# Optimization experiments

Hardware: AMD Instinct MI355X
Metric: run time of the kernel (lower is better)

## Reference

```python
import jax, jax.numpy as jnp
import numpy as np

B, N, M, D = 2, 256, 8, 256      # batch, seq, modalities, dmodel
H, DH = 8, 64                     # heads, dim_head (hardcoded defaults)
INNER = H * DH                    # 512
MULT = 4                          # FFN mult
SCALE = DH ** -0.5
EPS = 1e-5


def layer_norm(x, g, b):
    mu = jnp.mean(x, axis=-1, keepdims=True)
    var = jnp.mean((x - mu) ** 2, axis=-1, keepdims=True)
    return (x - mu) * jax.lax.rsqrt(var + EPS) * g + b


def setup_inputs() -> dict:
    key = jax.random.key(0)
    ks = jax.random.split(key, 8)
    s = 0.02
    return {
        "x": jax.random.normal(ks[0], (B, D, M, N), jnp.float32),
        "Wq": jax.random.normal(ks[1], (D, INNER), jnp.float32) * s,
        "Wkv": jax.random.normal(ks[2], (D, 2 * INNER), jnp.float32) * s,
        "Wout": jax.random.normal(ks[3], (INNER * M, D * M), jnp.float32) * s,
        "bout": jnp.zeros((D * M,), jnp.float32),
        "g1": jnp.ones((D,), jnp.float32),
        "beta1": jnp.zeros((D,), jnp.float32),
        "Wff1": jax.random.normal(ks[4], (D, 2 * D * MULT), jnp.float32) * s,
        "bff1": jnp.zeros((2 * D * MULT,), jnp.float32),
        "Wff2": jax.random.normal(ks[5], (D * MULT, D), jnp.float32) * s,
        "bff2": jnp.zeros((D,), jnp.float32),
        "g2": jnp.ones((D,), jnp.float32),
        "beta2": jnp.zeros((D,), jnp.float32),
    }


def reference(x, Wq, Wkv, Wout, bout, g1, beta1, Wff1, bff1, Wff2, bff2, g2, beta2):
    x_shape = x.shape
    xt = jnp.transpose(x, (0, 3, 2, 1))          # [B,N,M,D]
    # --- Channel_Seq_Big_Attention (self-attention, context = x) ---
    q = (xt @ Wq).reshape(B, N, M, H, DH)
    kv = xt @ Wkv
    k, v = jnp.split(kv, 2, axis=-1)
    k = k.reshape(B, N, M, H, DH)
    v = v.reshape(B, N, M, H, DH)
    # sim: [(b h), i, j, m, z] kept as [B,H,i,j,m,z]
    sim = jnp.einsum('bimhd,bjzhd->bhijmz', q, k) * SCALE
    attn = jax.nn.softmax(sim, axis=2)           # softmax over j (dim=-3 of bijmz)
    out = jnp.einsum('bhijmz,bjmhd->bizhd', attn, v)  # [B,N,M,H,DH]
    out = out.reshape(B, N, M * H * DH)          # 'b n (m h d)'
    o = (out @ Wout + bout).reshape(B, N, M, D)
    # --- residual + post-norm ---
    xt = layer_norm(xt + o, g1, beta1)
    # --- GEGLU FFN ---
    hg = xt @ Wff1 + bff1
    a, gate = jnp.split(hg, 2, axis=-1)
    ff = (a * jax.nn.gelu(gate, approximate=False)) @ Wff2 + bff2
    xt = layer_norm(xt + ff, g2, beta2)
    return xt.reshape(x_shape)                   # torch .view(x_shape)
```

## Files before the change

### kernel.cpp

```cpp
#include <hip/hip_runtime.h>
#include <math.h>

#define KS_ 0.1803368801111244f

typedef __attribute__((ext_vector_type(8))) short bf16x8;
typedef __attribute__((ext_vector_type(4))) short bf16x4;
typedef __attribute__((ext_vector_type(4))) float f32x4;

__device__ inline short f2bf(float f) {
  unsigned u = __builtin_bit_cast(unsigned, f);
  u += 0x7fff + ((u >> 16) & 1);
  return (short)(u >> 16);
}

__device__ inline void wt_tile(const float* __restrict__ W, short* __restrict__ WT,
                               int K, int N, int bx, int by, int t, float (*tile)[33]) {
  int n0 = bx * 32, k0 = by * 32;
  int tx = t & 31, ty = t >> 5;
#pragma unroll
  for (int r = 0; r < 32; r += 8)
    tile[ty + r][tx] = W[(size_t)(k0 + ty + r) * N + n0 + tx];
  __syncthreads();
#pragma unroll
  for (int r = 0; r < 32; r += 8)
    WT[(size_t)(n0 + ty + r) * K + k0 + tx] = f2bf(tile[tx][ty + r]);
}

__global__ __launch_bounds__(256) void k_prep_all(const float* __restrict__ x, float* __restrict__ xt,
                                                  short* __restrict__ xtbf,
                                                  const float* __restrict__ Wq, const float* __restrict__ Wkv,
                                                  const float* __restrict__ Wout, const float* __restrict__ Wff1,
                                                  const float* __restrict__ Wff2,
                                                  short* __restrict__ WqkvT, short* __restrict__ WoutT,
                                                  short* __restrict__ Wff1T, short* __restrict__ Wff2T) {
  __shared__ float tile[32][33];
  int bid = blockIdx.x, t = threadIdx.x;
  if (bid < 8192) {
    wt_tile(Wout, WoutT, 4096, 2048, bid & 63, bid >> 6, t, tile);
  } else if (bid < 9216) {
    int r = bid - 8192;
    int bx = r & 7, by = (r >> 3) & 7, bm = r >> 6;
    int b = bm >> 3, m = bm & 7;
    int d0 = bx * 32, n0 = by * 32;
    int tx = t & 31, ty = t >> 5;
#pragma unroll
    for (int rr = 0; rr < 32; rr += 8) {
      int d = d0 + ty + rr, n = n0 + tx;
      tile[ty + rr][tx] = x[((size_t)(b * 256 + d) * 8 + m) * 256 + n];
    }
    __syncthreads();
#pragma unroll
    for (int rr = 0; rr < 32; rr += 8) {
      int n = n0 + ty + rr, d = d0 + tx;
      float v = tile[tx][ty + rr];
      size_t idx = ((size_t)(b * 256 + n) * 8 + m) * 256 + d;
      xt[idx] = v;
      xtbf[idx] = f2bf(v);
    }
  } else if (bid < 9344) {
    int r = bid - 9216;
    wt_tile(Wq, WqkvT, 256, 512, r & 15, r >> 4, t, tile);
  } else if (bid < 9600) {
    int r = bid - 9344;
    wt_tile(Wkv, WqkvT + 131072, 256, 1024, r & 31, r >> 5, t, tile);
  } else if (bid < 10112) {
    int r = bid - 9600;
    wt_tile(Wff1, Wff1T, 256, 2048, r & 63, r >> 6, t, tile);
  } else {
    int r = bid - 10112;
    wt_tile(Wff2, Wff2T, 1024, 256, r & 7, r >> 3, t, tile);
  }
}

__global__ __launch_bounds__(256) void k_gemm_qkv(const short* __restrict__ A, const short* __restrict__ Bt,
                                                  short* __restrict__ qfrag, short* __restrict__ kfrag,
                                                  short* __restrict__ vfrag) {
  __shared__ short As[64 * 40];
  __shared__ short Bs[64 * 40];
  __shared__ short Cs[64 * 72];
  int t = threadIdx.x;
  int bx = blockIdx.x, by = blockIdx.y;
  int sel = bx >> 3, h = bx & 7;
  int row0 = by * 64, col0 = bx * 64;
  int b = by >> 5, n0 = (by * 8) & 255;
  int bh = b * 8 + h;
  int w = t >> 6, lane = t & 63, quad = lane >> 4, l16 = lane & 15;
  int wr = w >> 1, wc = w & 1;
  int lrow = t >> 2, lch = (t & 3) * 8;
  const short* Ap = A + (size_t)(row0 + lrow) * 256 + lch;
  const short* Bp = Bt + (size_t)(col0 + lrow) * 256 + lch;
  f32x4 acc[2][2] = {{{0,0,0,0},{0,0,0,0}},{{0,0,0,0},{0,0,0,0}}};
  bf16x8 av = *(const bf16x8*)(Ap);
  bf16x8 bv = *(const bf16x8*)(Bp);
  for (int k0 = 0; k0 < 256; k0 += 32) {
    *(bf16x8*)&As[lrow * 40 + lch] = av;
    *(bf16x8*)&Bs[lrow * 40 + lch] = bv;
    __syncthreads();
    if (k0 + 32 < 256) {
      av = *(const bf16x8*)(Ap + k0 + 32);
      bv = *(const bf16x8*)(Bp + k0 + 32);
    }
    bf16x8 af[2], bf[2];
#pragma unroll
    for (int rf = 0; rf < 2; rf++) af[rf] = *(const bf16x8*)&As[(wr * 32 + rf * 16 + l16) * 40 + quad * 8];
#pragma unroll
    for (int cf = 0; cf < 2; cf++) bf[cf] = *(const bf16x8*)&Bs[(wc * 32 + cf * 16 + l16) * 40 + quad * 8];
#pragma unroll
    for (int rf = 0; rf < 2; rf++)
#pragma unroll
      for (int cf = 0; cf < 2; cf++)
        acc[rf][cf] = __builtin_amdgcn_mfma_f32_16x16x32_bf16(af[rf], bf[cf], acc[rf][cf], 0, 0, 0);
    __syncthreads();
  }
  if (sel < 2) {
#pragma unroll
    for (int rf = 0; rf < 2; rf++)
#pragma unroll
      for (int cf = 0; cf < 2; cf++) {
        int col = wc * 32 + cf * 16 + l16;
#pragma unroll
        for (int r = 0; r < 4; r++)
          Cs[(wr * 32 + rf * 16 + quad * 4 + r) * 72 + col] = f2bf(acc[rf][cf][r]);
      }
  } else {
#pragma unroll
    for (int rf = 0; rf < 2; rf++)
#pragma unroll
      for (int cf = 0; cf < 2; cf++) {
        int col = wc * 32 + cf * 16 + l16;
        bf16x4 pk;
#pragma unroll
        for (int r = 0; r < 4; r++) pk[r] = f2bf(acc[rf][cf][r]);
        *(bf16x4*)&Cs[col * 72 + wr * 32 + rf * 16 + quad * 4] = pk;
      }
  }
  __syncthreads();
  if (sel < 2) {
    short* dst = sel ? kfrag : qfrag;
    int it = n0 >> 4, l16b = n0 & 8;
#pragma unroll
    for (int cidx = 0; cidx < 2; cidx++) {
      int chunk = t + cidx * 256;
      int m = chunk >> 6, ks2 = (chunk >> 5) & 1, q2 = (chunk >> 3) & 3, n = chunk & 7;
      bf16x8 val = *(const bf16x8*)&Cs[(n * 8 + m) * 72 + ks2 * 32 + q2 * 8];
      size_t off = ((size_t)(bh * 128 + m * 16 + it) * 2 + ks2) * 512 + (q2 * 16 + l16b + n) * 8;
      *(bf16x8*)(dst + off) = val;
    }
  } else {
    int jc = n0 >> 5, jf = (n0 >> 4) & 1, qbase = (n0 & 8) >> 2;
#pragma unroll
    for (int cidx = 0; cidx < 2; cidx++) {
      int chunk = t + cidx * 256;
      int qd = chunk >> 8, m0 = (chunk >> 6) & 3, dtt = (chunk >> 4) & 3, l16c = chunk & 15;
      int d = dtt * 16 + l16c;
      unsigned u[4];
#pragma unroll
      for (int e3 = 0; e3 < 4; e3++)
        u[e3] = *(const unsigned*)&Cs[d * 72 + qd * 32 + e3 * 8 + 2 * m0];
      uint4 pv;
      pv.x = __builtin_amdgcn_perm(u[1], u[0], 0x05040100u);
      pv.y = __builtin_amdgcn_perm(u[3], u[2], 0x05040100u);
      pv.z = __builtin_amdgcn_perm(u[1], u[0], 0x07060302u);
      pv.w = __builtin_amdgcn_perm(u[3], u[2], 0x07060302u);
      int quad2 = qbase + qd;
      size_t cid = (((size_t)(bh * 8 + jc) * 4 + m0) * 4 + dtt) * 2 + jf;
      *(bf16x8*)(vfrag + cid * 512 + (quad2 * 16 + l16c) * 8) = __builtin_bit_cast(bf16x8, pv);
    }
  }
}

__global__ __launch_bounds__(256) void k_gemm_bf(const short* __restrict__ A, const short* __restrict__ Bt,
                                                 const float* __restrict__ bias, float* __restrict__ C,
                                                 int M, int N, int K, int Ks) {
  __shared__ short As[64 * 40];
  __shared__ short Bs[64 * 40];
  int t = threadIdx.x;
  int row0 = blockIdx.y * 64, col0 = blockIdx.x * 64;
  int kp = blockIdx.z;
  int kbeg = kp * Ks, kend = kbeg + Ks;
  int w = t >> 6, lane = t & 63, quad = lane >> 4, l16 = lane & 15;
  int wr = w >> 1, wc = w & 1;
  int lrow = t >> 2, lch = (t & 3) * 8;
  const short* Ap = A + (size_t)(row0 + lrow) * K + lch;
  const short* Bp = Bt + (size_t)(col0 + lrow) * K + lch;
  f32x4 acc[2][2] = {{{0,0,0,0},{0,0,0,0}},{{0,0,0,0},{0,0,0,0}}};
  bf16x8 av = *(const bf16x8*)(Ap + kbeg);
  bf16x8 bv = *(const bf16x8*)(Bp + kbeg);
  for (int k0 = kbeg; k0 < kend; k0 += 32) {
    *(bf16x8*)&As[lrow * 40 + lch] = av;
    *(bf16x8*)&Bs[lrow * 40 + lch] = bv;
    __syncthreads();
    if (k0 + 32 < kend) {
      av = *(const bf16x8*)(Ap + k0 + 32);
      bv = *(const bf16x8*)(Bp + k0 + 32);
    }
    bf16x8 af[2], bf[2];
#pragma unroll
    for (int rf = 0; rf < 2; rf++) af[rf] = *(const bf16x8*)&As[(wr * 32 + rf * 16 + l16) * 40 + quad * 8];
#pragma unroll
    for (int cf = 0; cf < 2; cf++) bf[cf] = *(const bf16x8*)&Bs[(wc * 32 + cf * 16 + l16) * 40 + quad * 8];
#pragma unroll
    for (int rf = 0; rf < 2; rf++)
#pragma unroll
      for (int cf = 0; cf < 2; cf++)
        acc[rf][cf] = __builtin_amdgcn_mfma_f32_16x16x32_bf16(af[rf], bf[cf], acc[rf][cf], 0, 0, 0);
    __syncthreads();
  }
  float* Cp = C + (size_t)kp * M * N;
#pragma unroll
  for (int rf = 0; rf < 2; rf++)
#pragma unroll
    for (int cf = 0; cf < 2; cf++) {
      int col = col0 + wc * 32 + cf * 16 + l16;
      float vb = (bias && kp == 0) ? bias[col] : 0.0f;
#pragma unroll
      for (int r = 0; r < 4; r++) {
        int row = row0 + wr * 32 + rf * 16 + quad * 4 + r;
        Cp[(size_t)row * N + col] = acc[rf][cf][r] + vb;
      }
    }
}

__global__ __launch_bounds__(256) void k_ff1g(const short* __restrict__ A, const short* __restrict__ Bt,
                                              const float* __restrict__ bias, short* __restrict__ gg) {
  __shared__ short As[64 * 40];
  __shared__ short Ba[64 * 40];
  __shared__ short Bg[64 * 40];
  int t = threadIdx.x;
  int colA0 = blockIdx.x * 64, row0 = blockIdx.y * 64;
  int w = t >> 6, lane = t & 63, quad = lane >> 4, l16 = lane & 15;
  int wr = w >> 1, wc = w & 1;
  int lrow = t >> 2, lch = (t & 3) * 8;
  const short* Ap  = A + (size_t)(row0 + lrow) * 256 + lch;
  const short* Bpa = Bt + (size_t)(colA0 + lrow) * 256 + lch;
  const short* Bpg = Bt + (size_t)(1024 + colA0 + lrow) * 256 + lch;
  f32x4 za = {0, 0, 0, 0};
  f32x4 acc_a[2][2] = {{za, za}, {za, za}};
  f32x4 acc_g[2][2] = {{za, za}, {za, za}};
  bf16x8 av = *(const bf16x8*)(Ap);
  bf16x8 bva = *(const bf16x8*)(Bpa);
  bf16x8 bvg = *(const bf16x8*)(Bpg);
  for (int k0 = 0; k0 < 256; k0 += 32) {
    *(bf16x8*)&As[lrow * 40 + lch] = av;
    *(bf16x8*)&Ba[lrow * 40 + lch] = bva;
    *(bf16x8*)&Bg[lrow * 40 + lch] = bvg;
    __syncthreads();
    if (k0 + 32 < 256) {
      av  = *(const bf16x8*)(Ap + k0 + 32);
      bva = *(const bf16x8*)(Bpa + k0 + 32);
      bvg = *(const bf16x8*)(Bpg + k0 + 32);
    }
    bf16x8 af[2], ba[2], bg[2];
#pragma unroll
    for (int rf = 0; rf < 2; rf++) af[rf] = *(const bf16x8*)&As[(wr * 32 + rf * 16 + l16) * 40 + quad * 8];
#pragma unroll
    for (int cf = 0; cf < 2; cf++) {
      ba[cf] = *(const bf16x8*)&Ba[(wc * 32 + cf * 16 + l16) * 40 + quad * 8];
      bg[cf] = *(const bf16x8*)&Bg[(wc * 32 + cf * 16 + l16) * 40 + quad * 8];
    }
#pragma unroll
    for (int rf = 0; rf < 2; rf++)
#pragma unroll
      for (int cf = 0; cf < 2; cf++) {
        acc_a[rf][cf] = __builtin_amdgcn_mfma_f32_16x16x32_bf16(af[rf], ba[cf], acc_a[rf][cf], 0, 0, 0);
        acc_g[rf][cf] = __builtin_amdgcn_mfma_f32_16x16x32_bf16(af[rf], bg[cf], acc_g[rf][cf], 0, 0, 0);
      }
    __syncthreads();
  }
#pragma unroll
  for (int rf = 0; rf < 2; rf++)
#pragma unroll
    for (int cf = 0; cf < 2; cf++) {
      int col = colA0 + wc * 32 + cf * 16 + l16;
      float ba_ = bias[col], bg_ = bias[1024 + col];
#pragma unroll
      for (int r = 0; r < 4; r++) {
        int row = row0 + wr * 32 + rf * 16 + quad * 4 + r;
        float a = acc_a[rf][cf][r] + ba_;
        float g = acc_g[rf][cf][r] + bg_;
        float ge = 0.5f * g * (1.0f + erff(g * 0.70710678118654752f));
        gg[(size_t)row * 1024 + col] = f2bf(a * ge);
      }
    }
}

__global__ __launch_bounds__(256) void k_attn_den5(const short* __restrict__ qfrag, const short* __restrict__ kfrag,
                                                   float* __restrict__ rdg) {
  int ct2 = blockIdx.x, mp = blockIdx.y, bh = blockIdx.z;
  int t = threadIdx.x;
  int w = t >> 6, lane = t & 63;
  int rt0 = ct2 * 8 + w * 2;
  bf16x8 bfr[2][2];
#pragma unroll
  for (int cf = 0; cf < 2; cf++)
#pragma unroll
    for (int ks = 0; ks < 2; ks++)
      bfr[cf][ks] = *(const bf16x8*)(kfrag + ((size_t)((bh * 128 + rt0 + cf) * 2 + ks)) * 512 + lane * 8);
  for (int mi = 0; mi < 2; mi++) {
    int m = mp * 2 + mi;
    float fa0 = 0.0f, fa1 = 0.0f;
#pragma unroll 4
    for (int it2 = 0; it2 < 16; it2++) {
      const short* ap = qfrag + ((size_t)((bh * 128 + m * 16 + it2) * 2)) * 512 + lane * 8;
      bf16x8 a0 = *(const bf16x8*)ap;
      bf16x8 a1 = *(const bf16x8*)(ap + 512);
      f32x4 c0 = {0, 0, 0, 0}, c1 = {0, 0, 0, 0};
      c0 = __builtin_amdgcn_mfma_f32_16x16x32_bf16(a0, bfr[0][0], c0, 0, 0, 0);
      c0 = __builtin_amdgcn_mfma_f32_16x16x32_bf16(a1, bfr[0][1], c0, 0, 0, 0);
      c1 = __builtin_amdgcn_mfma_f32_16x16x32_bf16(a0, bfr[1][0], c1, 0, 0, 0);
      c1 = __builtin_amdgcn_mfma_f32_16x16x32_bf16(a1, bfr[1][1], c1, 0, 0, 0);
#pragma unroll
      for (int r = 0; r < 4; r++) {
        fa0 += __builtin_amdgcn_exp2f(c0[r] * KS_);
        fa1 += __builtin_amdgcn_exp2f(c1[r] * KS_);
      }
    }
    fa0 += __shfl_xor(fa0, 16); fa0 += __shfl_xor(fa0, 32);
    fa1 += __shfl_xor(fa1, 16); fa1 += __shfl_xor(fa1, 32);
    if (lane < 16) {
      rdg[(size_t)(bh * 8 + m) * 2048 + rt0 * 16 + lane] = -__builtin_amdgcn_logf(fa0);
      rdg[(size_t)(bh * 8 + m) * 2048 + (rt0 + 1) * 16 + lane] = -__builtin_amdgcn_logf(fa1);
    }
  }
}

__global__ __launch_bounds__(256) void k_attn_out6(const short* __restrict__ qfrag, const short* __restrict__ kfrag,
                                                   const short* __restrict__ vfrag, const float* __restrict__ rdg,
                                                   short* __restrict__ ao) {
  __shared__ float red[4 * 64 * 17];
  int z = blockIdx.x, itp = blockIdx.y, bh = blockIdx.z;
  int b = bh >> 3, h = bh & 7;
  int t = threadIdx.x, w = t >> 6, lane = t & 63, quad = lane >> 4, l16 = lane & 15;
  const float* rb = rdg + (size_t)bh * 16384;
  f32x4 z4 = {0, 0, 0, 0};
  bf16x8 qf[2][2][2];
#pragma unroll
  for (int iti = 0; iti < 2; iti++)
#pragma unroll
    for (int mm = 0; mm < 2; mm++)
#pragma unroll
      for (int ks = 0; ks < 2; ks++)
        qf[iti][mm][ks] = *(const bf16x8*)(qfrag +
            ((size_t)((bh * 128 + (2 * w + mm) * 16 + itp * 2 + iti) * 2 + ks)) * 512 + lane * 8);
  f32x4 acc[2][4];
#pragma unroll
  for (int iti = 0; iti < 2; iti++)
#pragma unroll
    for (int dt = 0; dt < 4; dt++) acc[iti][dt] = z4;
  bf16x8 vf[4][2], kf[2][2];
  float4 nv0[2], nv1[2];
#pragma unroll
  for (int dt = 0; dt < 4; dt++)
#pragma unroll
    for (int jf = 0; jf < 2; jf++)
      vf[dt][jf] = *(const bf16x8*)(vfrag + ((((size_t)(bh * 8 + 0) * 4 + w) * 4 + dt) * 2 + jf) * 512 + lane * 8);
#pragma unroll
  for (int jf = 0; jf < 2; jf++) {
    const short* kp = kfrag + ((size_t)((bh * 128 + z * 16 + 0 * 2 + jf) * 2)) * 512 + lane * 8;
    kf[jf][0] = *(const bf16x8*)kp;
    kf[jf][1] = *(const bf16x8*)(kp + 512);
    nv0[jf] = *(const float4*)(rb + (size_t)(2 * w) * 2048 + z * 256 + 0 * 32 + jf * 16 + quad * 4);
    nv1[jf] = *(const float4*)(rb + (size_t)(2 * w + 1) * 2048 + z * 256 + 0 * 32 + jf * 16 + quad * 4);
  }
  for (int jc = 0; jc < 8; jc++) {
    bf16x8 vfn[4][2], kfn[2][2];
    float4 nv0n[2], nv1n[2];
    if (jc < 7) {
      int jn = jc + 1;
#pragma unroll
      for (int dt = 0; dt < 4; dt++)
#pragma unroll
        for (int jf = 0; jf < 2; jf++)
          vfn[dt][jf] = *(const bf16x8*)(vfrag + ((((size_t)(bh * 8 + jn) * 4 + w) * 4 + dt) * 2 + jf) * 512 + lane * 8);
#pragma unroll
      for (int jf = 0; jf < 2; jf++) {
        const short* kp = kfrag + ((size_t)((bh * 128 + z * 16 + jn * 2 + jf) * 2)) * 512 + lane * 8;
        kfn[jf][0] = *(const bf16x8*)kp;
        kfn[jf][1] = *(const bf16x8*)(kp + 512);
        nv0n[jf] = *(const float4*)(rb + (size_t)(2 * w) * 2048 + z * 256 + jn * 32 + jf * 16 + quad * 4);
        nv1n[jf] = *(const float4*)(rb + (size_t)(2 * w + 1) * 2048 + z * 256 + jn * 32 + jf * 16 + quad * 4);
      }
    }
    float n0[2][4] = {{nv0[0].x, nv0[0].y, nv0[0].z, nv0[0].w}, {nv0[1].x, nv0[1].y, nv0[1].z, nv0[1].w}};
    float n1[2][4] = {{nv1[0].x, nv1[0].y, nv1[0].z, nv1[0].w}, {nv1[1].x, nv1[1].y, nv1[1].z, nv1[1].w}};
#pragma unroll
    for (int iti = 0; iti < 2; iti++) {
      f32x4 c[2][2] = {{z4, z4}, {z4, z4}};
#pragma unroll
      for (int jf = 0; jf < 2; jf++)
#pragma unroll
        for (int mm = 0; mm < 2; mm++) {
          c[jf][mm] = __builtin_amdgcn_mfma_f32_16x16x32_bf16(kf[jf][0], qf[iti][mm][0], c[jf][mm], 0, 0, 0);
          c[jf][mm] = __builtin_amdgcn_mfma_f32_16x16x32_bf16(kf[jf][1], qf[iti][mm][1], c[jf][mm], 0, 0, 0);
        }
      bf16x8 pf[2];
#pragma unroll
      for (int jf = 0; jf < 2; jf++) {
        unsigned u[8];
#pragma unroll
        for (int e = 0; e < 4; e++) {
          u[e]     = __builtin_bit_cast(unsigned, __builtin_amdgcn_exp2f(fmaf(c[jf][0][e], KS_, n0[jf][e]))) + 0x8000u;
          u[e + 4] = __builtin_bit_cast(unsigned, __builtin_amdgcn_exp2f(fmaf(c[jf][1][e], KS_, n1[jf][e]))) + 0x8000u;
        }
        uint4 pv;
        pv.x = __builtin_amdgcn_perm(u[1], u[0], 0x07060302u);
        pv.y = __builtin_amdgcn_perm(u[3], u[2], 0x07060302u);
        pv.z = __builtin_amdgcn_perm(u[5], u[4], 0x07060302u);
        pv.w = __builtin_amdgcn_perm(u[7], u[6], 0x07060302u);
        pf[jf] = __builtin_bit_cast(bf16x8, pv);
      }
#pragma unroll
      for (int dt = 0; dt < 4; dt++)
#pragma unroll
        for (int jf = 0; jf < 2; jf++)
          acc[iti][dt] = __builtin_amdgcn_mfma_f32_16x16x32_bf16(vf[dt][jf], pf[jf], acc[iti][dt], 0, 0, 0);
    }
    if (jc < 7) {
#pragma unroll
      for (int dt = 0; dt < 4; dt++)
#pragma unroll
        for (int jf = 0; jf < 2; jf++) vf[dt][jf] = vfn[dt][jf];
#pragma unroll
      for (int jf = 0; jf < 2; jf++) {
        kf[jf][0] = kfn[jf][0]; kf[jf][1] = kfn[jf][1];
        nv0[jf] = nv0n[jf]; nv1[jf] = nv1n[jf];
      }
    }
  }
  for (int iti = 0; iti < 2; iti++) {
#pragma unroll
    for (int dt = 0; dt < 4; dt++)
#pragma unroll
      for (int r = 0; r < 4; r++)
        red[w * 1088 + (dt * 16 + quad * 4 + r) * 17 + l16] = acc[iti][dt][r];
    __syncthreads();
    {
      int i = t >> 4, dg = t & 15;
      float s[4] = {0, 0, 0, 0};
#pragma unroll
      for (int w2 = 0; w2 < 4; w2++)
#pragma unroll
        for (int r2 = 0; r2 < 4; r2++)
          s[r2] += red[w2 * 1088 + (dg * 4 + r2) * 17 + i];
      bf16x4 ov;
#pragma unroll
      for (int r2 = 0; r2 < 4; r2++) ov[r2] = f2bf(s[r2]);
      *(bf16x4*)(ao + (size_t)((b * 256 + itp * 32 + iti * 16 + i) * 8 + z) * 512 + h * 64 + dg * 4) = ov;
    }
    __syncthreads();
  }
}

__global__ __launch_bounds__(256) void k_ln(const float* __restrict__ X, const float* __restrict__ P, int np,
                                            const float* __restrict__ g, const float* __restrict__ be,
                                            float* __restrict__ Y, short* __restrict__ Ybf) {
  __shared__ float sm[8];
  int row = blockIdx.x, t = threadIdx.x;
  int lane = t & 63, w = t >> 6;
  size_t base = (size_t)row * 256;
  float v = X[base + t];
  for (int p = 0; p < np; p++) v += P[(size_t)p * 1048576 + base + t];
  float s = v;
  s += __shfl_xor(s, 1); s += __shfl_xor(s, 2); s += __shfl_xor(s, 4);
  s += __shfl_xor(s, 8); s += __shfl_xor(s, 16); s += __shfl_xor(s, 32);
  if (lane == 0) sm[w] = s;
  __syncthreads();
  float mu = (sm[0] + sm[1] + sm[2] + sm[3]) * (1.0f / 256.0f);
  float dv = v - mu;
  float s2 = dv * dv;
  s2 += __shfl_xor(s2, 1); s2 += __shfl_xor(s2, 2); s2 += __shfl_xor(s2, 4);
  s2 += __shfl_xor(s2, 8); s2 += __shfl_xor(s2, 16); s2 += __shfl_xor(s2, 32);
  if (lane == 0) sm[4 + w] = s2;
  __syncthreads();
  float var = (sm[4] + sm[5] + sm[6] + sm[7]) * (1.0f / 256.0f);
  float rs = rsqrtf(var + 1e-5f);
  float res = dv * rs * g[t] + be[t];
  Y[base + t] = res;
  if (Ybf) Ybf[base + t] = f2bf(res);
}

extern "C" void kernel_launch(void* const* d_in, const int* in_sizes, int n_in,
                              void* d_out, int out_size, void* d_ws, size_t ws_size,
                              hipStream_t stream) {
  const float* x    = (const float*)d_in[0];
  const float* Wq   = (const float*)d_in[1];
  const float* Wkv  = (const float*)d_in[2];
  const float* Wout = (const float*)d_in[3];
  const float* bout = (const float*)d_in[4];
  const float* g1   = (const float*)d_in[5];
  const float* be1  = (const float*)d_in[6];
  const float* Wff1 = (const float*)d_in[7];
  const float* bff1 = (const float*)d_in[8];
  const float* Wff2 = (const float*)d_in[9];
  const float* bff2 = (const float*)d_in[10];
  const float* g2   = (const float*)d_in[11];
  const float* be2  = (const float*)d_in[12];
  float* out = (float*)d_out;
  float* w = (float*)d_ws;

  float* xt   = w;
  float* part = w + 1048576;
  float* y    = w + 9437184;
  float* rdg  = w + 11534336;
  short* sb     = (short*)(w + 11796480);
  short* qfrag  = sb;
  short* kfrag  = sb + 2097152;
  short* vfrag  = sb + 4194304;
  short* xt_bf  = sb + 6291456;
  short* ao_bf  = sb + 7340032;
  short* y_bf   = sb + 9437184;
  short* gg_bf  = sb + 10485760;
  short* WqkvT  = sb + 14680064;
  short* WoutT  = sb + 15073280;
  short* Wff1T  = sb + 23461888;
  short* Wff2T  = sb + 23986176;

  k_prep_all<<<10368, 256, 0, stream>>>(x, xt, xt_bf, Wq, Wkv, Wout, Wff1, Wff2,
                                        WqkvT, WoutT, Wff1T, Wff2T);
  k_gemm_qkv<<<dim3(24, 64), 256, 0, stream>>>(xt_bf, WqkvT, qfrag, kfrag, vfrag);
  k_attn_den5<<<dim3(16, 4, 16), 256, 0, stream>>>(qfrag, kfrag, rdg);
  k_attn_out6<<<dim3(8, 8, 16), 256, 0, stream>>>(qfrag, kfrag, vfrag, rdg, ao_bf);
  k_gemm_bf<<<dim3(32, 8, 4), 256, 0, stream>>>(ao_bf, WoutT, bout, part, 512, 2048, 4096, 1024);
  k_ln<<<4096, 256, 0, stream>>>(xt, part, 4, g1, be1, y, y_bf);
  k_ff1g<<<dim3(16, 64), 256, 0, stream>>>(y_bf, Wff1T, bff1, gg_bf);
  k_gemm_bf<<<dim3(4, 64, 4), 256, 0, stream>>>(gg_bf, Wff2T, bff2, part, 4096, 256, 1024, 256);
  k_ln<<<4096, 256, 0, stream>>>(y, part, 4, g2, be2, out, nullptr);
}
```

Baseline: 220.8 us.

## Use direct global-to-LDS loads with XOR-swizzled double-buffered tiles in GEMMs

Replaces the register-staged global loads and LDS stores in the three bf16 GEMM kernels (qkv, generic, ff1 GEGLU) with global_load_lds 16-byte async copies into double-buffered LDS tiles. The padded 40-stride layout becomes a dense 32-stride layout with an XOR chunk swizzle to avoid bank conflicts on the MFMA fragment reads. One barrier per k-step is removed and the VGPR staging goes away. The cost is doubled LDS per block, and correctness now depends on the wave-contiguous LDS destination ordering of global_load_lds and on its completion being ensured before the barrier.

```diff
diff --git a/kernel.cpp b/kernel.cpp
--- a/kernel.cpp
+++ b/kernel.cpp
@@ -11,6 +11,12 @@
   unsigned u = __builtin_bit_cast(unsigned, f);
   u += 0x7fff + ((u >> 16) & 1);
   return (short)(u >> 16);
+}
+
+__device__ inline void gload16(const short* g, short* l) {
+  __builtin_amdgcn_global_load_lds(
+      (const __attribute__((address_space(1))) void*)g,
+      (__attribute__((address_space(3))) void*)l, 16, 0, 0);
 }
 
 __device__ inline void wt_tile(const float* __restrict__ W, short* __restrict__ WT,
@@ -75,8 +81,8 @@
 __global__ __launch_bounds__(256) void k_gemm_qkv(const short* __restrict__ A, const short* __restrict__ Bt,
                                                   short* __restrict__ qfrag, short* __restrict__ kfrag,
                                                   short* __restrict__ vfrag) {
-  __shared__ short As[64 * 40];
-  __shared__ short Bs[64 * 40];
+  __shared__ short As[2][2048];
+  __shared__ short Bs[2][2048];
   __shared__ short Cs[64 * 72];
   int t = threadIdx.x;
   int bx = blockIdx.x, by = blockIdx.y;
@@ -86,31 +92,41 @@
   int bh = b * 8 + h;
   int w = t >> 6, lane = t & 63, quad = lane >> 4, l16 = lane & 15;
   int wr = w >> 1, wc = w & 1;
-  int lrow = t >> 2, lch = (t & 3) * 8;
-  const short* Ap = A + (size_t)(row0 + lrow) * 256 + lch;
-  const short* Bp = Bt + (size_t)(col0 + lrow) * 256 + lch;
+  int r = t >> 2;
+  int cs = ((t & 3) ^ ((r >> 1) & 3)) * 8;
+  const short* Ag = A + (size_t)(row0 + r) * 256 + cs;
+  const short* Bg = Bt + (size_t)(col0 + r) * 256 + cs;
+  int sw = (l16 >> 1) & 3;
+  int chk = (quad ^ sw) * 8;
+  int aoff[2], boff[2];
+#pragma unroll
+  for (int rf = 0; rf < 2; rf++) {
+    aoff[rf] = (wr * 32 + rf * 16 + l16) * 32 + chk;
+    boff[rf] = (wc * 32 + rf * 16 + l16) * 32 + chk;
+  }
   f32x4 acc[2][2] = {{{0,0,0,0},{0,0,0,0}},{{0,0,0,0},{0,0,0,0}}};
-  bf16x8 av = *(const bf16x8*)(Ap);
-  bf16x8 bv = *(const bf16x8*)(Bp);
+  gload16(Ag, &As[0][w * 512]);
+  gload16(Bg, &Bs[0][w * 512]);
+  __syncthreads();
+  int buf = 0;
   for (int k0 = 0; k0 < 256; k0 += 32) {
-    *(bf16x8*)&As[lrow * 40 + lch] = av;
-    *(bf16x8*)&Bs[lrow * 40 + lch] = bv;
-    __syncthreads();
+    int nb = buf ^ 1;
     if (k0 + 32 < 256) {
-      av = *(const bf16x8*)(Ap + k0 + 32);
-      bv = *(const bf16x8*)(Bp + k0 + 32);
+      gload16(Ag + k0 + 32, &As[nb][w * 512]);
+      gload16(Bg + k0 + 32, &Bs[nb][w * 512]);
     }
     bf16x8 af[2], bf[2];
 #pragma unroll
-    for (int rf = 0; rf < 2; rf++) af[rf] = *(const bf16x8*)&As[(wr * 32 + rf * 16 + l16) * 40 + quad * 8];
-#pragma unroll
-    for (int cf = 0; cf < 2; cf++) bf[cf] = *(const bf16x8*)&Bs[(wc * 32 + cf * 16 + l16) * 40 + quad * 8];
+    for (int rf = 0; rf < 2; rf++) af[rf] = *(const bf16x8*)&As[buf][aoff[rf]];
+#pragma unroll
+    for (int cf = 0; cf < 2; cf++) bf[cf] = *(const bf16x8*)&Bs[buf][boff[cf]];
 #pragma unroll
     for (int rf = 0; rf < 2; rf++)
 #pragma unroll
       for (int cf = 0; cf < 2; cf++)
         acc[rf][cf] = __builtin_amdgcn_mfma_f32_16x16x32_bf16(af[rf], bf[cf], acc[rf][cf], 0, 0, 0);
     __syncthreads();
+    buf = nb;
   }
   if (sel < 2) {
 #pragma unroll
@@ -119,8 +135,8 @@
       for (int cf = 0; cf < 2; cf++) {
         int col = wc * 32 + cf * 16 + l16;
 #pragma unroll
-        for (int r = 0; r < 4; r++)
-          Cs[(wr * 32 + rf * 16 + quad * 4 + r) * 72 + col] = f2bf(acc[rf][cf][r]);
+        for (int rr = 0; rr < 4; rr++)
+          Cs[(wr * 32 + rf * 16 + quad * 4 + rr) * 72 + col] = f2bf(acc[rf][cf][rr]);
       }
   } else {
 #pragma unroll
@@ -130,7 +146,7 @@
         int col = wc * 32 + cf * 16 + l16;
         bf16x4 pk;
 #pragma unroll
-        for (int r = 0; r < 4; r++) pk[r] = f2bf(acc[rf][cf][r]);
+        for (int rr = 0; rr < 4; rr++) pk[rr] = f2bf(acc[rf][cf][rr]);
         *(bf16x4*)&Cs[col * 72 + wr * 32 + rf * 16 + quad * 4] = pk;
       }
   }
@@ -172,39 +188,49 @@
 __global__ __launch_bounds__(256) void k_gemm_bf(const short* __restrict__ A, const short* __restrict__ Bt,
                                                  const float* __restrict__ bias, float* __restrict__ C,
                                                  int M, int N, int K, int Ks) {
-  __shared__ short As[64 * 40];
-  __shared__ short Bs[64 * 40];
+  __shared__ short As[2][2048];
+  __shared__ short Bs[2][2048];
   int t = threadIdx.x;
   int row0 = blockIdx.y * 64, col0 = blockIdx.x * 64;
   int kp = blockIdx.z;
   int kbeg = kp * Ks, kend = kbeg + Ks;
   int w = t >> 6, lane = t & 63, quad = lane >> 4, l16 = lane & 15;
   int wr = w >> 1, wc = w & 1;
-  int lrow = t >> 2, lch = (t & 3) * 8;
-  const short* Ap = A + (size_t)(row0 + lrow) * K + lch;
-  const short* Bp = Bt + (size_t)(col0 + lrow) * K + lch;
+  int r = t >> 2;
+  int cs = ((t & 3) ^ ((r >> 1) & 3)) * 8;
+  const short* Ag = A + (size_t)(row0 + r) * K + cs;
+  const short* Bg = Bt + (size_t)(col0 + r) * K + cs;
+  int sw = (l16 >> 1) & 3;
+  int chk = (quad ^ sw) * 8;
+  int aoff[2], boff[2];
+#pragma unroll
+  for (int rf = 0; rf < 2; rf++) {
+    aoff[rf] = (wr * 32 + rf * 16 + l16) * 32 + chk;
+    boff[rf] = (wc * 32 + rf * 16 + l16) * 32 + chk;
+  }
   f32x4 acc[2][2] = {{{0,0,0,0},{0,0,0,0}},{{0,0,0,0},{0,0,0,0}}};
-  bf16x8 av = *(const bf16x8*)(Ap + kbeg);
-  bf16x8 bv = *(const bf16x8*)(Bp + kbeg);
+  gload16(Ag + kbeg, &As[0][w * 512]);
+  gload16(Bg + kbeg, &Bs[0][w * 512]);
+  __syncthreads();
+  int buf = 0;
   for (int k0 = kbeg; k0 < kend; k0 += 32) {
-    *(bf16x8*)&As[lrow * 40 + lch] = av;
-    *(bf16x8*)&Bs[lrow * 40 + lch] = bv;
-    __syncthreads();
+    int nb = buf ^ 1;
     if (k0 + 32 < kend) {
-      av = *(const bf16x8*)(Ap + k0 + 32);
-      bv = *(const bf16x8*)(Bp + k0 + 32);
+      gload16(Ag + k0 + 32, &As[nb][w * 512]);
+      gload16(Bg + k0 + 32, &Bs[nb][w * 512]);
     }
     bf16x8 af[2], bf[2];
 #pragma unroll
-    for (int rf = 0; rf < 2; rf++) af[rf] = *(const bf16x8*)&As[(wr * 32 + rf * 16 + l16) * 40 + quad * 8];
-#pragma unroll
-    for (int cf = 0; cf < 2; cf++) bf[cf] = *(const bf16x8*)&Bs[(wc * 32 + cf * 16 + l16) * 40 + quad * 8];
+    for (int rf = 0; rf < 2; rf++) af[rf] = *(const bf16x8*)&As[buf][aoff[rf]];
+#pragma unroll
+    for (int cf = 0; cf < 2; cf++) bf[cf] = *(const bf16x8*)&Bs[buf][boff[cf]];
 #pragma unroll
     for (int rf = 0; rf < 2; rf++)
 #pragma unroll
       for (int cf = 0; cf < 2; cf++)
         acc[rf][cf] = __builtin_amdgcn_mfma_f32_16x16x32_bf16(af[rf], bf[cf], acc[rf][cf], 0, 0, 0);
     __syncthreads();
+    buf = nb;
   }
   float* Cp = C + (size_t)kp * M * N;
 #pragma unroll
@@ -214,49 +240,57 @@
       int col = col0 + wc * 32 + cf * 16 + l16;
       float vb = (bias && kp == 0) ? bias[col] : 0.0f;
 #pragma unroll
-      for (int r = 0; r < 4; r++) {
-        int row = row0 + wr * 32 + rf * 16 + quad * 4 + r;
-        Cp[(size_t)row * N + col] = acc[rf][cf][r] + vb;
+      for (int rr = 0; rr < 4; rr++) {
+        int row = row0 + wr * 32 + rf * 16 + quad * 4 + rr;
+        Cp[(size_t)row * N + col] = acc[rf][cf][rr] + vb;
       }
     }
 }
 
 __global__ __launch_bounds__(256) void k_ff1g(const short* __restrict__ A, const short* __restrict__ Bt,
                                               const float* __restrict__ bias, short* __restrict__ gg) {
-  __shared__ short As[64 * 40];
-  __shared__ short Ba[64 * 40];
-  __shared__ short Bg[64 * 40];
+  __shared__ short As[2][2048];
+  __shared__ short Ba[2][2048];
+  __shared__ short Bgs[2][2048];
   int t = threadIdx.x;
   int colA0 = blockIdx.x * 64, row0 = blockIdx.y * 64;
   int w = t >> 6, lane = t & 63, quad = lane >> 4, l16 = lane & 15;
   int wr = w >> 1, wc = w & 1;
-  int lrow = t >> 2, lch = (t & 3) * 8;
-  const short* Ap  = A + (size_t)(row0 + lrow) * 256 + lch;
-  const short* Bpa = Bt + (size_t)(colA0 + lrow) * 256 + lch;
-  const short* Bpg = Bt + (size_t)(1024 + colA0 + lrow) * 256 + lch;
+  int r = t >> 2;
+  int cs = ((t & 3) ^ ((r >> 1) & 3)) * 8;
+  const short* Ag  = A + (size_t)(row0 + r) * 256 + cs;
+  const short* Bpa = Bt + (size_t)(colA0 + r) * 256 + cs;
+  const short* Bpg = Bt + (size_t)(1024 + colA0 + r) * 256 + cs;
+  int sw = (l16 >> 1) & 3;
+  int chk = (quad ^ sw) * 8;
+  int aoff[2], boff[2];
+#pragma unroll
+  for (int rf = 0; rf < 2; rf++) {
+    aoff[rf] = (wr * 32 + rf * 16 + l16) * 32 + chk;
+    boff[rf] = (wc * 32 + rf * 16 + l16) * 32 + chk;
+  }
   f32x4 za = {0, 0, 0, 0};
   f32x4 acc_a[2][2] = {{za, za}, {za, za}};
   f32x4 acc_g[2][2] = {{za, za}, {za, za}};
-  bf16x8 av = *(const bf16x8*)(Ap);
-  bf16x8 bva = *(const bf16x8*)(Bpa);
-  bf16x8 bvg = *(const bf16x8*)(Bpg);
+  gload16(Ag, &As[0][w * 512]);
+  gload16(Bpa, &Ba[0][w * 512]);
+  gload16(Bpg, &Bgs[0][w * 512]);
+  __syncthreads();
+  int buf = 0;
   for (int k0 = 0; k0 < 256; k0 += 32) {
-    *(bf16x8*)&As[lrow * 40 + lch] = av;
-    *(bf16x8*)&Ba[lrow * 40 + lch] = bva;
-    *(bf16x8*)&Bg[lrow * 40 + lch] = bvg;
-    __syncthreads();
+    int nb = buf ^ 1;
     if (k0 + 32 < 256) {
-      av  = *(const bf16x8*)(Ap + k0 + 32);
-      bva = *(const bf16x8*)(Bpa + k0 + 32);
-      bvg = *(const bf16x8*)(Bpg + k0 + 32);
+      gload16(Ag + k0 + 32, &As[nb][w * 512]);
+      gload16(Bpa + k0 + 32, &Ba[nb][w * 512]);
+      gload16(Bpg + k0 + 32, &Bgs[nb][w * 512]);
     }
     bf16x8 af[2], ba[2], bg[2];
 #pragma unroll
-    for (int rf = 0; rf < 2; rf++) af[rf] = *(const bf16x8*)&As[(wr * 32 + rf * 16 + l16) * 40 + quad * 8];
+    for (int rf = 0; rf < 2; rf++) af[rf] = *(const bf16x8*)&As[buf][aoff[rf]];
 #pragma unroll
     for (int cf = 0; cf < 2; cf++) {
-      ba[cf] = *(const bf16x8*)&Ba[(wc * 32 + cf * 16 + l16) * 40 + quad * 8];
-      bg[cf] = *(const bf16x8*)&Bg[(wc * 32 + cf * 16 + l16) * 40 + quad * 8];
+      ba[cf] = *(const bf16x8*)&Ba[buf][boff[cf]];
+      bg[cf] = *(const bf16x8*)&Bgs[buf][boff[cf]];
     }
 #pragma unroll
     for (int rf = 0; rf < 2; rf++)
@@ -266,6 +300,7 @@
         acc_g[rf][cf] = __builtin_amdgcn_mfma_f32_16x16x32_bf16(af[rf], bg[cf], acc_g[rf][cf], 0, 0, 0);
       }
     __syncthreads();
+    buf = nb;
   }
 #pragma unroll
   for (int rf = 0; rf < 2; rf++)
@@ -274,10 +309,10 @@
       int col = colA0 + wc * 32 + cf * 16 + l16;
       float ba_ = bias[col], bg_ = bias[1024 + col];
 #pragma unroll
-      for (int r = 0; r < 4; r++) {
-        int row = row0 + wr * 32 + rf * 16 + quad * 4 + r;
-        float a = acc_a[rf][cf][r] + ba_;
-        float g = acc_g[rf][cf][r] + bg_;
+      for (int rr = 0; rr < 4; rr++) {
+        int row = row0 + wr * 32 + rf * 16 + quad * 4 + rr;
+        float a = acc_a[rf][cf][rr] + ba_;
+        float g = acc_g[rf][cf][rr] + bg_;
         float ge = 0.5f * g * (1.0f + erff(g * 0.70710678118654752f));
         gg[(size_t)row * 1024 + col] = f2bf(a * ge);
       }
@@ -310,9 +345,9 @@
       c1 = __builtin_amdgcn_mfma_f32_16x16x32_bf16(a0, bfr[1][0], c1, 0, 0, 0);
       c1 = __builtin_amdgcn_mfma_f32_16x16x32_bf16(a1, bfr[1][1], c1, 0, 0, 0);
 #pragma unroll
-      for (int r = 0; r < 4; r++) {
-        fa0 += __builtin_amdgcn_exp2f(c0[r] * KS_);
-        fa1 += __builtin_amdgcn_exp2f(c1[r] * KS_);
+      for (int rr = 0; rr < 4; rr++) {
+        fa0 += __builtin_amdgcn_exp2f(c0[rr] * KS_);
+        fa1 += __builtin_amdgcn_exp2f(c1[rr] * KS_);
       }
     }
     fa0 += __shfl_xor(fa0, 16); fa0 += __shfl_xor(fa0, 32);
@@ -431,8 +466,8 @@
 #pragma unroll
     for (int dt = 0; dt < 4; dt++)
 #pragma unroll
-      for (int r = 0; r < 4; r++)
-        red[w * 1088 + (dt * 16 + quad * 4 + r) * 17 + l16] = acc[iti][dt][r];
+      for (int rr = 0; rr < 4; rr++)
+        red[w * 1088 + (dt * 16 + quad * 4 + rr) * 17 + l16] = acc[iti][dt][rr];
     __syncthreads();
     {
       int i = t >> 4, dg = t & 15;
```

After: 217.7 us. No clear change (-1.4%).
